# Performance work log

Measured on AMD Instinct MI355X. Metric: run time of the kernel, lower is better.

Reference implementation:

```python
import jax, jax.numpy as jnp
import numpy as np

N = 100000      # nodes
E = 1600000     # edges (avg degree 16)
IN = 128        # in_channels
H = 128         # hidden_channels
EPS = 1e-5      # BatchNorm eps


def setup_inputs() -> dict:
    key = jax.random.key(0)
    ks = jax.random.split(key, 10)
    x = jax.random.normal(ks[0], (N, IN), jnp.float32)
    edge_index = jax.random.randint(ks[1], (2, E), 0, N, dtype=jnp.int32)

    def lin(k, i, o):
        return jax.random.normal(k, (i, o), jnp.float32) * (1.0 / np.sqrt(i))

    d2 = 2 * H
    return {
        "x": x, "edge_index": edge_index,
        # SAGEConv 1: 128 -> 128
        "w1l": lin(ks[2], IN, H), "w1r": lin(ks[3], IN, H), "b1": jnp.zeros((H,), jnp.float32),
        "g1": jnp.ones((H,), jnp.float32), "be1": jnp.zeros((H,), jnp.float32),
        "m1": jnp.zeros((H,), jnp.float32), "v1": jnp.ones((H,), jnp.float32),
        # SAGEConv 2: 128 -> 256
        "w2l": lin(ks[4], H, d2), "w2r": lin(ks[5], H, d2), "b2": jnp.zeros((d2,), jnp.float32),
        "g2": jnp.ones((d2,), jnp.float32), "be2": jnp.zeros((d2,), jnp.float32),
        "m2": jnp.zeros((d2,), jnp.float32), "v2": jnp.ones((d2,), jnp.float32),
        # SAGEConv 3: 256 -> 256
        "w3l": lin(ks[6], d2, d2), "w3r": lin(ks[7], d2, d2), "b3": jnp.zeros((d2,), jnp.float32),
        "g3": jnp.ones((d2,), jnp.float32), "be3": jnp.zeros((d2,), jnp.float32),
        "m3": jnp.zeros((d2,), jnp.float32), "v3": jnp.ones((d2,), jnp.float32),
    }


def _sage_conv(x, src, dst, wl, wr, b):
    # PyG SAGEConv (mean aggr): out = mean_{j in N(i)} x_j @ W_l + x_i @ W_r + b
    agg = jax.ops.segment_sum(x[src], dst, num_segments=N)          # [N, d_in]
    deg = jax.ops.segment_sum(jnp.ones((src.shape[0],), x.dtype), dst, num_segments=N)
    mean = agg / jnp.maximum(deg, 1.0)[:, None]
    return mean @ wl + x @ wr + b


def _bn(x, g, b, m, v):
    # BatchNorm1d in eval mode (running stats); dropout is a no-op in eval
    return (x - m) * jax.lax.rsqrt(v + EPS) * g + b


def reference(x, edge_index,
              w1l, w1r, b1, g1, be1, m1, v1,
              w2l, w2r, b2, g2, be2, m2, v2,
              w3l, w3r, b3, g3, be3, m3, v3):
    src, dst = edge_index[0], edge_index[1]
    h = _bn(jax.nn.relu(_sage_conv(x, src, dst, w1l, w1r, b1)), g1, be1, m1, v1)
    h = _bn(jax.nn.relu(_sage_conv(h, src, dst, w2l, w2r, b2)), g2, be2, m2, v2)
    h = _bn(jax.nn.relu(_sage_conv(h, src, dst, w3l, w3r, b3)), g3, be3, m3, v3)
    return h  # [N, 2*H]
```

## Files before the change

kernel.cpp:

```cpp
#include <hip/hip_runtime.h>

#define NNODES 100000
#define NEDGES 1600000
#define EPSV 1e-5f

#define NB   391
#define BCAP 4608
#define EPB  4096

typedef __attribute__((ext_vector_type(8))) short bf16x8;
typedef __attribute__((ext_vector_type(4))) float f32x4;
typedef __attribute__((ext_vector_type(2))) float f32x2;

#if defined(__has_builtin)
#  if __has_builtin(__builtin_amdgcn_cvt_pk_f32_fp8) && __has_builtin(__builtin_amdgcn_cvt_pk_fp8_f32)
#    define HAS_FP8_CVT 1
#  endif
#endif
#ifndef HAS_FP8_CVT
#  define HAS_FP8_CVT 0
#endif

__device__ __forceinline__ ushort f2bf(float f) {
    union { float f; uint u; } c; c.f = f;
    uint u = c.u;
    return (ushort)((u + 0x7fffu + ((u >> 16) & 1u)) >> 16);
}
__device__ __forceinline__ uint pack2(float f0, float f1) {
    return (uint)f2bf(f0) | ((uint)f2bf(f1) << 16);
}

#if !HAS_FP8_CVT
__device__ __forceinline__ float fp8_dec1(uint b) {
    uint e = (b >> 3) & 0xFu, m = b & 7u, s = b >> 7;
    union { uint u; float f; } c;
    c.u = e ? ((s << 31) | ((e + 120u) << 23) | (m << 20)) : (s << 31);
    return c.f;
}
__device__ __forceinline__ uint fp8_enc1(float x) {
    union { float f; uint u; } c; c.f = x;
    uint u = c.u, s = u >> 31;
    float ax = fabsf(x);
    if (ax < 0.015625f) return s << 7;
    if (ax > 448.0f)    return (s << 7) | 0x7Eu;
    u = u + 0x7FFFFu + ((u >> 20) & 1u);
    uint e = ((u >> 23) & 0xFFu) - 120u;
    uint m = (u >> 20) & 7u;
    if (e > 15u) return (s << 7) | 0x7Eu;
    return (s << 7) | (e << 3) | m;
}
#endif

__device__ __forceinline__ void accf8p(f32x2* a, uint2 v) {
#if HAS_FP8_CVT
    a[0] += __builtin_amdgcn_cvt_pk_f32_fp8((int)v.x, false);
    a[1] += __builtin_amdgcn_cvt_pk_f32_fp8((int)v.x, true);
    a[2] += __builtin_amdgcn_cvt_pk_f32_fp8((int)v.y, false);
    a[3] += __builtin_amdgcn_cvt_pk_f32_fp8((int)v.y, true);
#else
    a[0] += (f32x2){fp8_dec1(v.x & 0xFFu), fp8_dec1((v.x >> 8) & 0xFFu)};
    a[1] += (f32x2){fp8_dec1((v.x >> 16) & 0xFFu), fp8_dec1(v.x >> 24)};
    a[2] += (f32x2){fp8_dec1(v.y & 0xFFu), fp8_dec1((v.y >> 8) & 0xFFu)};
    a[3] += (f32x2){fp8_dec1((v.y >> 16) & 0xFFu), fp8_dec1(v.y >> 24)};
#endif
}

__device__ __forceinline__ uint f2fp8(float f) {
#if HAS_FP8_CVT
    return ((uint)__builtin_amdgcn_cvt_pk_fp8_f32(f, f, 0, false)) & 0xFFu;
#else
    return fp8_enc1(f);
#endif
}

__device__ __forceinline__ uint packf8_4(float f0, float f1, float f2, float f3) {
#if HAS_FP8_CVT
    int r = 0;
    r = __builtin_amdgcn_cvt_pk_fp8_f32(f0, f1, r, false);
    r = __builtin_amdgcn_cvt_pk_fp8_f32(f2, f3, r, true);
    return (uint)r;
#else
    return fp8_enc1(f0) | (fp8_enc1(f1) << 8) | (fp8_enc1(f2) << 16) | (fp8_enc1(f3) << 24);
#endif
}

__device__ __forceinline__ void load_lds16(const ushort* g, ushort* l) {
    __builtin_amdgcn_global_load_lds(
        (const __attribute__((address_space(1))) void*)g,
        (__attribute__((address_space(3))) void*)l,
        16, 0, 0);
}

__global__ __launch_bounds__(256) void part_kernel(
    const int* __restrict__ src, const int* __restrict__ dst,
    int* __restrict__ cursor, uint2* __restrict__ pairs, int E)
{
    __shared__ int lcnt[NB];
    __shared__ int lbase[NB];
    const int t = threadIdx.x;
    for (int i = t; i < NB; i += 256) lcnt[i] = 0;
    __syncthreads();

    const int base = blockIdx.x * EPB;
    const int lim  = min(base + EPB, E);

    for (int e = base + t; e < lim; e += 256)
        atomicAdd(&lcnt[((unsigned)dst[e]) >> 8], 1);
    __syncthreads();

    for (int i = t; i < NB; i += 256) {
        int c = lcnt[i];
        lbase[i] = c ? atomicAdd(&cursor[i], c) : 0;
        lcnt[i] = 0;
    }
    __syncthreads();

    for (int e = base + t; e < lim; e += 256) {
        int d = dst[e];
        int b = ((unsigned)d) >> 8;
        int p = lbase[b] + atomicAdd(&lcnt[b], 1);
        if (p < BCAP) pairs[(size_t)b * BCAP + p] = make_uint2((uint)src[e], (uint)d);
    }
}

__global__ __launch_bounds__(512) void bscan_kernel(const int* __restrict__ cursor,
                                                    int* __restrict__ colBase)
{
    __shared__ int s[512];
    int t = threadIdx.x;
    int v = (t < NB) ? min(cursor[t], BCAP) : 0;
    s[t] = v;
    __syncthreads();
    #pragma unroll
    for (int off = 1; off < 512; off <<= 1) {
        int a = (t >= off) ? s[t - off] : 0;
        __syncthreads();
        s[t] += a;
        __syncthreads();
    }
    if (t < NB) colBase[t] = s[t] - v;
}

__global__ __launch_bounds__(256) void csr_fin_kernel(
    const uint2* __restrict__ pairs, const int* __restrict__ cursor,
    const int* __restrict__ colBase, uint2* __restrict__ meta,
    int* __restrict__ col, int n)
{
    __shared__ int lcnt[256];
    __shared__ int lofs[256];
    const int b = blockIdx.x;
    const int t = threadIdx.x;
    const int ecnt  = min(cursor[b], BCAP);
    const int cbase = colBase[b];
    const uint2* __restrict__ pp = pairs + (size_t)b * BCAP;

    lcnt[t] = 0;
    __syncthreads();
    for (int e = t; e < ecnt; e += 256)
        atomicAdd(&lcnt[pp[e].y & 255u], 1);
    __syncthreads();

    const int v = lcnt[t];
    lofs[t] = v;
    __syncthreads();
    #pragma unroll
    for (int off = 1; off < 256; off <<= 1) {
        int a = (t >= off) ? lofs[t - off] : 0;
        __syncthreads();
        lofs[t] += a;
        __syncthreads();
    }
    const int excl = lofs[t] - v;

    const int node = (b << 8) + t;
    if (node < n)
        meta[node] = make_uint2((uint)(cbase + excl), (uint)v);
    __syncthreads();
    lcnt[t] = excl;
    __syncthreads();

    for (int e = t; e < ecnt; e += 256) {
        uint2 pr = pp[e];
        int p = cbase + atomicAdd(&lcnt[pr.y & 255u], 1);
        col[p] = (int)pr.x;
    }
}

__global__ void cvt_x_kernel(const float* __restrict__ in, ushort* __restrict__ outb,
                             unsigned char* __restrict__ out8, int n4) {
    int i = blockIdx.x * blockDim.x + threadIdx.x;
    if (i < n4) {
        float4 v = ((const float4*)in)[i];
        ushort4 o;
        o.x = f2bf(v.x); o.y = f2bf(v.y); o.z = f2bf(v.z); o.w = f2bf(v.w);
        ((ushort4*)outb)[i] = o;
        ((uint*)out8)[i] = packf8_4(v.x, v.y, v.z, v.w);
    }
}

__global__ void wT_all_kernel(
    const float* __restrict__ w1l, const float* __restrict__ w1r,
    const float* __restrict__ w2l, const float* __restrict__ w2r,
    const float* __restrict__ w3l, const float* __restrict__ w3r,
    ushort* __restrict__ t1l, ushort* __restrict__ t1r,
    ushort* __restrict__ t2l, ushort* __restrict__ t2r,
    ushort* __restrict__ t3l, ushort* __restrict__ t3r)
{
    int idx = blockIdx.x * blockDim.x + threadIdx.x;
    const float* w; ushort* wt; int K, Nout, i;
    if      (idx <  16384) { w = w1l; wt = t1l; K = 128; Nout = 128; i = idx; }
    else if (idx <  32768) { w = w1r; wt = t1r; K = 128; Nout = 128; i = idx - 16384; }
    else if (idx <  65536) { w = w2l; wt = t2l; K = 128; Nout = 256; i = idx - 32768; }
    else if (idx <  98304) { w = w2r; wt = t2r; K = 128; Nout = 256; i = idx - 65536; }
    else if (idx < 163840) { w = w3l; wt = t3l; K = 256; Nout = 256; i = idx - 98304; }
    else if (idx < 229376) { w = w3r; wt = t3r; K = 256; Nout = 256; i = idx - 163840; }
    else return;
    int k = i / Nout, n = i - k * Nout;
    wt[(size_t)n * K + k] = f2bf(w[i]);
}

template<int D>
__global__ __launch_bounds__(256) void gather_f8(
    const unsigned char* __restrict__ x, const uint2* __restrict__ meta,
    const int* __restrict__ col, ushort* __restrict__ agg, int n)
{
    constexpr int TPN = D / 8;
    constexpr int NPB = 256 / TPN;
    const int node = blockIdx.x * NPB + threadIdx.x / TPN;
    const int lane = threadIdx.x % TPN;
    if (node >= n) return;

    const uint2 m  = meta[node];
    const int  c   = (int)m.y;
    int        e   = (int)m.x;
    const int  end = e + c;
    const uint boff = (uint)lane * 8u;

    f32x2 a[4];
    #pragma unroll
    for (int i = 0; i < 4; ++i) a[i] = (f32x2)0.0f;

    while (e + 15 < end) {
        uint2 r[16];
        #pragma unroll
        for (int i = 0; i < 16; ++i)
            r[i] = *(const uint2*)(x + (uint)col[e + i] * (uint)D + boff);
        #pragma unroll
        for (int i = 0; i < 16; ++i) accf8p(a, r[i]);
        e += 16;
    }
    if (e + 7 < end) {
        uint2 r[8];
        #pragma unroll
        for (int i = 0; i < 8; ++i)
            r[i] = *(const uint2*)(x + (uint)col[e + i] * (uint)D + boff);
        #pragma unroll
        for (int i = 0; i < 8; ++i) accf8p(a, r[i]);
        e += 8;
    }
    for (; e + 1 < end; e += 2) {
        uint2 v0 = *(const uint2*)(x + (uint)col[e]     * (uint)D + boff);
        uint2 v1 = *(const uint2*)(x + (uint)col[e + 1] * (uint)D + boff);
        accf8p(a, v0); accf8p(a, v1);
    }
    if (e < end) {
        uint2 v = *(const uint2*)(x + (uint)col[e] * (uint)D + boff);
        accf8p(a, v);
    }

    const float inv = 1.0f / fmaxf((float)c, 1.0f);
    uint4 o;
    o.x = pack2(a[0][0] * inv, a[0][1] * inv);
    o.y = pack2(a[1][0] * inv, a[1][1] * inv);
    o.z = pack2(a[2][0] * inv, a[2][1] * inv);
    o.w = pack2(a[3][0] * inv, a[3][1] * inv);
    ((uint4*)agg)[(size_t)node * TPN + lane] = o;
}

template<int DIN, int DOUT, bool OUTF32, bool WRITE8>
__global__ __launch_bounds__(256) void mfma_layer(
    const ushort* __restrict__ xin, const ushort* __restrict__ agg,
    const ushort* __restrict__ wlT, const ushort* __restrict__ wrT,
    const float* __restrict__ bias, const float* __restrict__ gamma,
    const float* __restrict__ beta, const float* __restrict__ rmean,
    const float* __restrict__ rvar, void* __restrict__ outp,
    unsigned char* __restrict__ out8, int M)
{
    constexpr int BM = 128, BN = 128, BK = 64;
    constexpr int NBY = DOUT / BN;
    __shared__ ushort As[BM * BK];
    __shared__ ushort Bs[BN * BK];

    const int tid  = threadIdx.x;
    const int lane = tid & 63;
    const int wid  = tid >> 6;
    const int wm   = (wid & 1) * 64;
    const int wn   = (wid >> 1) * 64;
    const int lr   = lane & 15;
    const int quad = lane >> 4;

    const int row0 = (blockIdx.x / NBY) * BM;
    const int col0 = (blockIdx.x % NBY) * BN;

    f32x4 acc[4][4] = {};

    const int srow = tid >> 3;
    const int schk = (tid & 7) ^ (srow & 7);

    #pragma unroll
    for (int phase = 0; phase < 2; ++phase) {
        const ushort* __restrict__ A = phase ? xin : agg;
        const ushort* __restrict__ W = phase ? wrT : wlT;

        for (int k0 = 0; k0 < DIN; k0 += BK) {
            __syncthreads();
            #pragma unroll
            for (int r = 0; r < 4; ++r) {
                const int row = srow + r * 32;
                int gra = row0 + row; gra = gra < M ? gra : M - 1;
                load_lds16(A + (size_t)gra * DIN + k0 + schk * 8,
                           &As[(r * 256 + tid) * 8]);
                load_lds16(W + (size_t)(col0 + row) * DIN + k0 + schk * 8,
                           &Bs[(r * 256 + tid) * 8]);
            }
            __syncthreads();

            #pragma unroll
            for (int sub = 0; sub < 2; ++sub) {
                bf16x8 af[4], bf[4];
                #pragma unroll
                for (int t = 0; t < 4; ++t) {
                    const int ra = wm + t * 16 + lr;
                    const int rb = wn + t * 16 + lr;
                    const int ca = ((sub << 2) | quad) ^ (ra & 7);
                    const int cb = ((sub << 2) | quad) ^ (rb & 7);
                    af[t] = *(const bf16x8*)&As[ra * BK + ca * 8];
                    bf[t] = *(const bf16x8*)&Bs[rb * BK + cb * 8];
                }
                #pragma unroll
                for (int mt = 0; mt < 4; ++mt)
                    #pragma unroll
                    for (int nt = 0; nt < 4; ++nt)
                        acc[mt][nt] = __builtin_amdgcn_mfma_f32_16x16x32_bf16(
                            af[mt], bf[nt], acc[mt][nt], 0, 0, 0);
            }
        }
    }

    float bj[4], sj[4], mj[4], bej[4];
    #pragma unroll
    for (int nt = 0; nt < 4; ++nt) {
        int gc = col0 + wn + nt * 16 + lr;
        bj[nt]  = bias[gc];
        sj[nt]  = rsqrtf(rvar[gc] + EPSV) * gamma[gc];
        mj[nt]  = rmean[gc];
        bej[nt] = beta[gc];
    }
    #pragma unroll
    for (int mt = 0; mt < 4; ++mt) {
        #pragma unroll
        for (int r = 0; r < 4; ++r) {
            int grow = row0 + wm + mt * 16 + quad * 4 + r;
            if (grow < M) {
                #pragma unroll
                for (int nt = 0; nt < 4; ++nt) {
                    int gc = col0 + wn + nt * 16 + lr;
                    float h = acc[mt][nt][r] + bj[nt];
                    h = fmaxf(h, 0.0f);
                    h = (h - mj[nt]) * sj[nt] + bej[nt];
                    if (OUTF32) ((float*)outp)[(size_t)grow * DOUT + gc] = h;
                    else        ((ushort*)outp)[(size_t)grow * DOUT + gc] = f2bf(h);
                    if (WRITE8) out8[(size_t)grow * DOUT + gc] = (unsigned char)f2fp8(h);
                }
            }
        }
    }
}

extern "C" void kernel_launch(void* const* d_in, const int* in_sizes, int n_in,
                              void* d_out, int out_size, void* d_ws, size_t ws_size,
                              hipStream_t stream) {
    const int N = NNODES;
    const int E = NEDGES;

    const float* x   = (const float*)d_in[0];
    const int*   ei  = (const int*)d_in[1];
    const int*   src = ei;
    const int*   dst = ei + E;

    const float* w1l = (const float*)d_in[2];
    const float* w1r = (const float*)d_in[3];
    const float* b1  = (const float*)d_in[4];
    const float* g1  = (const float*)d_in[5];
    const float* be1 = (const float*)d_in[6];
    const float* m1  = (const float*)d_in[7];
    const float* v1  = (const float*)d_in[8];

    const float* w2l = (const float*)d_in[9];
    const float* w2r = (const float*)d_in[10];
    const float* b2  = (const float*)d_in[11];
    const float* g2  = (const float*)d_in[12];
    const float* be2 = (const float*)d_in[13];
    const float* m2  = (const float*)d_in[14];
    const float* v2  = (const float*)d_in[15];

    const float* w3l = (const float*)d_in[16];
    const float* w3r = (const float*)d_in[17];
    const float* b3  = (const float*)d_in[18];
    const float* g3  = (const float*)d_in[19];
    const float* be3 = (const float*)d_in[20];
    const float* m3  = (const float*)d_in[21];
    const float* v3  = (const float*)d_in[22];

    float* out = (float*)d_out;

    char*   wp      = (char*)d_ws;
    uint2*  meta    = (uint2*)wp;   wp += (size_t)N * sizeof(uint2);
    int*    cursor  = (int*)wp;     wp += 512 * sizeof(int);
    int*    colBase = (int*)wp;     wp += 512 * sizeof(int);
    int*    col     = (int*)wp;     wp += (size_t)E * sizeof(int);
    uint2*  pairs   = (uint2*)wp;   wp += (size_t)NB * BCAP * sizeof(uint2);
    ushort* xbf     = (ushort*)wp;  wp += (size_t)N * 128 * sizeof(ushort);
    ushort* h1      = (ushort*)wp;  wp += (size_t)N * 128 * sizeof(ushort);
    ushort* h2      = (ushort*)wp;  wp += (size_t)N * 256 * sizeof(ushort);
    ushort* aggb    = (ushort*)wp;  wp += (size_t)N * 256 * sizeof(ushort);
    unsigned char* h2f8 = (unsigned char*)wp; wp += (size_t)N * 256;
    ushort* w1lT    = (ushort*)wp;  wp += 128 * 128 * sizeof(ushort);
    ushort* w1rT    = (ushort*)wp;  wp += 128 * 128 * sizeof(ushort);
    ushort* w2lT    = (ushort*)wp;  wp += 256 * 128 * sizeof(ushort);
    ushort* w2rT    = (ushort*)wp;  wp += 256 * 128 * sizeof(ushort);
    ushort* w3lT    = (ushort*)wp;  wp += 256 * 256 * sizeof(ushort);
    ushort* w3rT    = (ushort*)wp;

    unsigned char* xf8  = (unsigned char*)pairs;
    unsigned char* h1f8 = (unsigned char*)pairs;

    const int T = 256;

    hipMemsetAsync(cursor, 0, 512 * sizeof(int), stream);
    part_kernel<<<(E + EPB - 1) / EPB, 256, 0, stream>>>(src, dst, cursor, pairs, E);
    bscan_kernel<<<1, 512, 0, stream>>>(cursor, colBase);
    csr_fin_kernel<<<NB, 256, 0, stream>>>(pairs, cursor, colBase, meta, col, N);

    cvt_x_kernel<<<((N * 128 / 4) + T - 1) / T, T, 0, stream>>>(x, xbf, xf8, N * 128 / 4);
    wT_all_kernel<<<229376 / 256, 256, 0, stream>>>(w1l, w1r, w2l, w2r, w3l, w3r,
                                                    w1lT, w1rT, w2lT, w2rT, w3lT, w3rT);

    const int nrb = (N + 127) / 128;

    gather_f8<128><<<(N + 15) / 16, 256, 0, stream>>>(xf8, meta, col, aggb, N);
    mfma_layer<128, 128, false, true><<<nrb * 1, 256, 0, stream>>>(
        xbf, aggb, w1lT, w1rT, b1, g1, be1, m1, v1, h1, h1f8, N);

    gather_f8<128><<<(N + 15) / 16, 256, 0, stream>>>(h1f8, meta, col, aggb, N);
    mfma_layer<128, 256, false, true><<<nrb * 2, 256, 0, stream>>>(
        h1, aggb, w2lT, w2rT, b2, g2, be2, m2, v2, h2, h2f8, N);

    gather_f8<256><<<(N + 7) / 8, 256, 0, stream>>>(h2f8, meta, col, aggb, N);
    mfma_layer<256, 256, true, false><<<nrb * 2, 256, 0, stream>>>(
        h2, aggb, w3lT, w3rT, b3, g3, be3, m3, v3, out, nullptr, N);
}
```

Baseline: 480.9 us.

## Store FP8 features in 32-column slabs and gather per slab

The FP8 feature copies are now stored as column slabs of 32 bytes per node, each slab contiguous across all nodes. The gather kernel is split so each block handles one slab for 64 nodes, which shrinks the random-access working set per pass so it fits better in L2/MALL cache. The cost is that neighbour indices are re-read once per slab, each random read touches only 32 bytes, and the FP8 stores in the MFMA epilogue become more scattered. The unroll depth also drops from 16 to 8.

After: 540.4 us. 1.12x slower.

```diff
diff --git a/kernel.cpp b/kernel.cpp
--- a/kernel.cpp
+++ b/kernel.cpp
@@ -194,7 +194,11 @@
         ushort4 o;
         o.x = f2bf(v.x); o.y = f2bf(v.y); o.z = f2bf(v.z); o.w = f2bf(v.w);
         ((ushort4*)outb)[i] = o;
-        ((uint*)out8)[i] = packf8_4(v.x, v.y, v.z, v.w);
+        uint byte = 4u * (uint)i;
+        uint nd   = byte >> 7;
+        uint b    = byte & 127u;
+        uint idx  = (b >> 5) * ((uint)NNODES * 8u) + nd * 8u + ((b & 31u) >> 2);
+        ((uint*)out8)[idx] = packf8_4(v.x, v.y, v.z, v.w);
     }
 }
 
@@ -220,51 +224,57 @@
 }
 
 template<int D>
-__global__ __launch_bounds__(256) void gather_f8(
+__global__ __launch_bounds__(256) void gather_f8s(
     const unsigned char* __restrict__ x, const uint2* __restrict__ meta,
     const int* __restrict__ col, ushort* __restrict__ agg, int n)
 {
-    constexpr int TPN = D / 8;
-    constexpr int NPB = 256 / TPN;
-    const int node = blockIdx.x * NPB + threadIdx.x / TPN;
-    const int lane = threadIdx.x % TPN;
+    constexpr int NS  = D / 32;
+    constexpr int NPB = 64;
+    const int s    = blockIdx.x % NS;
+    const int nb   = blockIdx.x / NS;
+    const int node = nb * NPB + (threadIdx.x >> 2);
+    const int lane = threadIdx.x & 3;
     if (node >= n) return;
+
+    const unsigned char* __restrict__ xs = x + (size_t)s * ((size_t)NNODES * 32);
+    const uint boff = (uint)lane * 8u;
 
     const uint2 m  = meta[node];
     const int  c   = (int)m.y;
     int        e   = (int)m.x;
     const int  end = e + c;
-    const uint boff = (uint)lane * 8u;
 
     f32x2 a[4];
     #pragma unroll
     for (int i = 0; i < 4; ++i) a[i] = (f32x2)0.0f;
 
-    while (e + 15 < end) {
-        uint2 r[16];
-        #pragma unroll
-        for (int i = 0; i < 16; ++i)
-            r[i] = *(const uint2*)(x + (uint)col[e + i] * (uint)D + boff);
-        #pragma unroll
-        for (int i = 0; i < 16; ++i) accf8p(a, r[i]);
-        e += 16;
-    }
-    if (e + 7 < end) {
-        uint2 r[8];
-        #pragma unroll
-        for (int i = 0; i < 8; ++i)
-            r[i] = *(const uint2*)(x + (uint)col[e + i] * (uint)D + boff);
-        #pragma unroll
-        for (int i = 0; i < 8; ++i) accf8p(a, r[i]);
-        e += 8;
+    for (; e + 7 < end; e += 8) {
+        uint o0 = ((uint)col[e]     << 5) + boff;
+        uint o1 = ((uint)col[e + 1] << 5) + boff;
+        uint o2 = ((uint)col[e + 2] << 5) + boff;
+        uint o3 = ((uint)col[e + 3] << 5) + boff;
+        uint o4 = ((uint)col[e + 4] << 5) + boff;
+        uint o5 = ((uint)col[e + 5] << 5) + boff;
+        uint o6 = ((uint)col[e + 6] << 5) + boff;
+        uint o7 = ((uint)col[e + 7] << 5) + boff;
+        uint2 v0 = *(const uint2*)(xs + o0);
+        uint2 v1 = *(const uint2*)(xs + o1);
+        uint2 v2 = *(const uint2*)(xs + o2);
+        uint2 v3 = *(const uint2*)(xs + o3);
+        uint2 v4 = *(const uint2*)(xs + o4);
+        uint2 v5 = *(const uint2*)(xs + o5);
+        uint2 v6 = *(const uint2*)(xs + o6);
+        uint2 v7 = *(const uint2*)(xs + o7);
+        accf8p(a, v0); accf8p(a, v1); accf8p(a, v2); accf8p(a, v3);
+        accf8p(a, v4); accf8p(a, v5); accf8p(a, v6); accf8p(a, v7);
     }
     for (; e + 1 < end; e += 2) {
-        uint2 v0 = *(const uint2*)(x + (uint)col[e]     * (uint)D + boff);
-        uint2 v1 = *(const uint2*)(x + (uint)col[e + 1] * (uint)D + boff);
+        uint2 v0 = *(const uint2*)(xs + ((uint)col[e]     << 5) + boff);
+        uint2 v1 = *(const uint2*)(xs + ((uint)col[e + 1] << 5) + boff);
         accf8p(a, v0); accf8p(a, v1);
     }
     if (e < end) {
-        uint2 v = *(const uint2*)(x + (uint)col[e] * (uint)D + boff);
+        uint2 v = *(const uint2*)(xs + ((uint)col[e] << 5) + boff);
         accf8p(a, v);
     }
 
@@ -274,7 +284,7 @@
     o.y = pack2(a[1][0] * inv, a[1][1] * inv);
     o.z = pack2(a[2][0] * inv, a[2][1] * inv);
     o.w = pack2(a[3][0] * inv, a[3][1] * inv);
-    ((uint4*)agg)[(size_t)node * TPN + lane] = o;
+    ((uint4*)agg)[(size_t)node * (D / 8) + s * 4 + lane] = o;
 }
 
 template<int DIN, int DOUT, bool OUTF32, bool WRITE8>
@@ -370,7 +380,10 @@
                     h = (h - mj[nt]) * sj[nt] + bej[nt];
                     if (OUTF32) ((float*)outp)[(size_t)grow * DOUT + gc] = h;
                     else        ((ushort*)outp)[(size_t)grow * DOUT + gc] = f2bf(h);
-                    if (WRITE8) out8[(size_t)grow * DOUT + gc] = (unsigned char)f2fp8(h);
+                    if (WRITE8)
+                        out8[(size_t)(gc >> 5) * ((size_t)NNODES * 32)
+                             + (size_t)grow * 32 + (gc & 31)] =
+                            (unsigned char)f2fp8(h);
                 }
             }
         }
@@ -447,16 +460,17 @@
                                                     w1lT, w1rT, w2lT, w2rT, w3lT, w3rT);
 
     const int nrb = (N + 127) / 128;
-
-    gather_f8<128><<<(N + 15) / 16, 256, 0, stream>>>(xf8, meta, col, aggb, N);
+    const int gnb = (N + 63) / 64;
+
+    gather_f8s<128><<<gnb * 4, 256, 0, stream>>>(xf8, meta, col, aggb, N);
     mfma_layer<128, 128, false, true><<<nrb * 1, 256, 0, stream>>>(
         xbf, aggb, w1lT, w1rT, b1, g1, be1, m1, v1, h1, h1f8, N);
 
-    gather_f8<128><<<(N + 15) / 16, 256, 0, stream>>>(h1f8, meta, col, aggb, N);
+    gather_f8s<128><<<gnb * 4, 256, 0, stream>>>(h1f8, meta, col, aggb, N);
     mfma_layer<128, 256, false, true><<<nrb * 2, 256, 0, stream>>>(
         h1, aggb, w2lT, w2rT, b2, g2, be2, m2, v2, h2, h2f8, N);
 
-    gather_f8<256><<<(N + 7) / 8, 256, 0, stream>>>(h2f8, meta, col, aggb, N);
+    gather_f8s<256><<<gnb * 8, 256, 0, stream>>>(h2f8, meta, col, aggb, N);
     mfma_layer<256, 256, true, false><<<nrb * 2, 256, 0, stream>>>(
         h2, aggb, w3lT, w3rT, b3, g3, be3, m3, v3, out, nullptr, N);
 }
```
